# Optimization experiments

Measured on AMD Instinct MI355X. Metric: run time of the kernel, lower is better.

The kernel has to match this reference:

```python
import jax, jax.numpy as jnp
import numpy as np

N, F, E, G, NNZ = 16000, 128, 256000, 512, 512000


def _hconv(xin, row, col, hw_passed, W, b, n_nodes, n_edges):
    """PyG HypergraphConv (use_attention=False), faithful to the repo's call.
    xin: [n_nodes, Fin]; row=hyper_edge[0] (graph-edge ids), col=hyper_edge[1] (hyperedge ids).
    hw_passed: [NNZ] -- the repo passes node_weight[hyper_edge[1]]; PyG then indexes it
    again by hyperedge_index[1], so the effective per-incidence weight is hw_passed[col].
    """
    xw = xin @ W                                   # lin(x), bias=False in PyG
    w = hw_passed[col]                             # [NNZ]
    D = jax.ops.segment_sum(w, row, num_segments=n_nodes)
    Dinv = jnp.where(D == 0, 0.0, 1.0 / jnp.where(D == 0, 1.0, D))
    Bdeg = jax.ops.segment_sum(jnp.ones(row.shape, xw.dtype), col, num_segments=n_edges)
    Binv = jnp.where(Bdeg == 0, 0.0, 1.0 / jnp.where(Bdeg == 0, 1.0, Bdeg))
    # node -> hyperedge: message = B[col] * xw[row], sum over col
    out_e = jax.ops.segment_sum(Binv[col][:, None] * xw[row], col, num_segments=n_edges)
    # hyperedge -> node: message = D[row] * out_e[col], sum over row
    out = jax.ops.segment_sum(Dinv[row][:, None] * out_e[col], row, num_segments=n_nodes)
    return out + b


def setup_inputs() -> dict:
    key = jax.random.key(0)
    ks = jax.random.split(key, 20)
    rn = lambda k, shape, s=0.05: jax.random.normal(k, shape, dtype=jnp.float32) * s
    return {
        "x": jax.random.normal(ks[0], (N, F), dtype=jnp.float32),
        "graph_emb": jax.random.normal(ks[1], (G, F), dtype=jnp.float32),
        "edge_index": jax.random.randint(ks[2], (2, E), 0, N),
        "edge_type": jax.random.randint(ks[3], (E,), 0, 8),
        "batch": jnp.sort(jax.random.randint(ks[4], (N,), 0, G)),
        "hyper_edge": jnp.concatenate([
            jax.random.randint(ks[5], (1, NNZ), 0, E),   # graph-edge ids
            jax.random.randint(ks[6], (1, NNZ), 0, N)],  # hyperedge ids
            axis=0),
        # HyperWeight.lin: 2F -> F -> 1
        "hw_w1": rn(ks[7], (2 * F, F)), "hw_b1": jnp.zeros((F,), jnp.float32),
        "hw_w2": rn(ks[8], (F, 1)), "hw_b2": jnp.zeros((1,), jnp.float32),
        # HypergraphConv 1: 2F -> 2F; 2: 2F -> F (lin bias=False, separate out bias)
        "c1_w": rn(ks[9], (2 * F, 2 * F)), "c1_b": jnp.zeros((2 * F,), jnp.float32),
        "c2_w": rn(ks[10], (2 * F, F)), "c2_b": jnp.zeros((F,), jnp.float32),
        # Generator.lin: 3F -> 4F -> F
        "g_w1": rn(ks[11], (3 * F, 4 * F)), "g_b1": jnp.zeros((4 * F,), jnp.float32),
        "g_w2": rn(ks[12], (4 * F, F)), "g_b2": jnp.zeros((F,), jnp.float32),
        # classifier: 2F -> F -> 1
        "cl_w1": rn(ks[13], (2 * F, F)), "cl_b1": jnp.zeros((F,), jnp.float32),
        "cl_w2": rn(ks[14], (F, 1)), "cl_b2": jnp.zeros((1,), jnp.float32),
        "attn": jnp.array([0.5, 0.5], jnp.float32),
    }


def reference(x, graph_emb, edge_index, edge_type, batch, hyper_edge,
              hw_w1, hw_b1, hw_w2, hw_b2, c1_w, c1_b, c2_w, c2_b,
              g_w1, g_b1, g_w2, g_b2, cl_w1, cl_b1, cl_w2, cl_b2, attn):
    col, row = edge_index[0], edge_index[1]
    xij0 = jnp.concatenate([x[col], x[row]], axis=-1)          # [E, 2F]
    gemb = graph_emb[batch[edge_index[0]]]                     # [E, F] (unbatch_gemb)
    proto = graph_emb[batch]                                   # [N, F]
    # HyperWeight: per-node scalar weight
    h = jax.nn.relu(jnp.concatenate([x, proto], axis=-1) @ hw_w1 + hw_b1)
    node_w = jax.nn.sigmoid(h @ hw_w2 + hw_b2)[:, 0]           # [N]
    hrow, hcol = hyper_edge[0], hyper_edge[1]
    hw_passed = node_w[hcol]                                   # [NNZ], as in repo
    er = jax.nn.sigmoid(_hconv(xij0, hrow, hcol, hw_passed, c1_w, c1_b, E, N))
    sij = jax.nn.sigmoid(_hconv(er, hrow, hcol, hw_passed, c2_w, c2_b, E, N))  # [E, F]
    # Generator.lin on [xij, gemb]
    xl = jax.nn.relu(jnp.concatenate([xij0, gemb], axis=-1) @ g_w1 + g_b1)
    xl = jax.nn.relu(xl @ g_w2 + g_b2)                         # [E, F]
    s = attn[0] * xl + attn[1] * sij
    s = jnp.concatenate([s, gemb], axis=-1)                    # [E, 2F]
    s = jax.nn.relu(s @ cl_w1 + cl_b1)
    sij_out = jax.nn.sigmoid(s @ cl_w2 + cl_b2)                # [E, 1] (eval mode)
    return sij_out
```

## Files before the change

### kernel.cpp

```cpp
#include <hip/hip_runtime.h>
#include <hip/hip_bf16.h>
#include <hip/hip_fp16.h>

#define NODES  16000
#define FDIM   128
#define EDGES  256000
#define NNZ_   512000

typedef __attribute__((ext_vector_type(8))) short bf16x8;
typedef __attribute__((ext_vector_type(8))) _Float16 f16x8;
typedef __attribute__((ext_vector_type(4))) float f32x4;

__device__ __forceinline__ float sigmoidf_(float z) { return 1.f / (1.f + __expf(-z)); }
__device__ __forceinline__ float bflo(unsigned u) { return __uint_as_float(u << 16); }
__device__ __forceinline__ float bfhi(unsigned u) { return __uint_as_float(u & 0xffff0000u); }
__device__ __forceinline__ unsigned pack2(float lo, float hi) {
    __hip_bfloat162 h;
    h.x = __float2bfloat16(lo);
    h.y = __float2bfloat16(hi);
    return *(unsigned*)&h;
}
__device__ __forceinline__ unsigned pk_add_f16(unsigned a, unsigned b) {
    unsigned r; asm("v_pk_add_f16 %0, %1, %2" : "=v"(r) : "v"(a), "v"(b)); return r;
}
__device__ __forceinline__ unsigned pk_relu_f16(unsigned a) {
    unsigned r; asm("v_pk_max_f16 %0, %1, %2" : "=v"(r) : "v"(a), "v"(0u)); return r;
}
__device__ __forceinline__ unsigned pkh(float lo, float hi) {
    __half2 h = __floats2half2_rn(lo, hi);
    return *(unsigned*)&h;
}
__device__ __forceinline__ float2 h2f2(unsigned u) {
    return __half22float2(*(__half2*)&u);
}

__global__ __launch_bounds__(128) void hyperweight_k(
    const float* __restrict__ x, const float* __restrict__ ge, const int* __restrict__ batch,
    const float* __restrict__ w1, const float* __restrict__ b1,
    const float* __restrict__ w2, const float* __restrict__ b2, float* __restrict__ node_w)
{
    __shared__ float a[8][256];
    __shared__ float red[128];
    const int t = threadIdx.x;
    const int nb = blockIdx.x * 8;
    for (int u = 0; u < 8; ++u) {
        int n = nb + u;
        a[u][t]       = x[(size_t)n * FDIM + t];
        a[u][128 + t] = ge[(size_t)batch[n] * FDIM + t];
    }
    __syncthreads();
    float acc[8] = {0,0,0,0,0,0,0,0};
    for (int k = 0; k < 256; ++k) {
        float wv = w1[k * 128 + t];
        #pragma unroll
        for (int u = 0; u < 8; ++u) acc[u] += a[u][k] * wv;
    }
    const float wv2 = w2[t];
    for (int u = 0; u < 8; ++u) {
        float h = fmaxf(acc[u] + b1[t], 0.f);
        red[t] = h * wv2;
        __syncthreads();
        for (int s2 = 64; s2 > 0; s2 >>= 1) {
            if (t < s2) red[t] += red[t + s2];
            __syncthreads();
        }
        if (t == 0) node_w[nb + u] = sigmoidf_(red[0] + b2[0]);
        __syncthreads();
    }
}

__global__ void incidence_pass(const int* __restrict__ he, const float* __restrict__ node_w,
                               float* __restrict__ D, int* __restrict__ Bcnt, int* __restrict__ rowCnt)
{
    int i = blockIdx.x * 256 + threadIdx.x;
    if (i >= NNZ_) return;
    int hr = he[i];
    int hc = he[NNZ_ + i];
    int hc2 = he[NNZ_ + hc];
    atomicAdd(&D[hr], node_w[hc2]);
    atomicAdd(&Bcnt[hc], 1);
    atomicAdd(&rowCnt[hr], 1);
}

__global__ void inv_k(float* __restrict__ D, const int* __restrict__ Bcnt, float* __restrict__ Binv) {
    int i = blockIdx.x * 256 + threadIdx.x;
    if (i < EDGES) {
        float d = D[i];
        D[i] = (d != 0.f) ? 1.f / d : 0.f;
    }
    if (i < NODES) {
        int c = Bcnt[i];
        Binv[i] = c ? 1.f / (float)c : 0.f;
    }
}

__global__ __launch_bounds__(1024) void reduce_chunks(const int* __restrict__ in, int* __restrict__ part, int n) {
    __shared__ int s[1024];
    int t = threadIdx.x, g = blockIdx.x * 1024 + t;
    s[t] = (g < n) ? in[g] : 0;
    __syncthreads();
    for (int d = 512; d > 0; d >>= 1) {
        if (t < d) s[t] += s[t + d];
        __syncthreads();
    }
    if (t == 0) part[blockIdx.x] = s[0];
}
__global__ __launch_bounds__(1024) void scan_sums(int* __restrict__ part, int nc) {
    __shared__ int s[1024];
    int t = threadIdx.x;
    int v = (t < nc) ? part[t] : 0;
    s[t] = v;
    __syncthreads();
    for (int d = 1; d < 1024; d <<= 1) {
        int tv = (t >= d) ? s[t - d] : 0;
        __syncthreads();
        s[t] += tv;
        __syncthreads();
    }
    if (t < nc) part[t] = s[t] - v;
}
__global__ __launch_bounds__(1024) void scan_chunks(const int* __restrict__ in, const int* __restrict__ part,
                                                    int* __restrict__ out, int n) {
    __shared__ int s[1024];
    int t = threadIdx.x, g = blockIdx.x * 1024 + t;
    int v = (g < n) ? in[g] : 0;
    s[t] = v;
    __syncthreads();
    for (int d = 1; d < 1024; d <<= 1) {
        int tv = (t >= d) ? s[t - d] : 0;
        __syncthreads();
        s[t] += tv;
        __syncthreads();
    }
    int excl = s[t] - v + part[blockIdx.x];
    if (g < n) out[g] = excl;
    if (g == n - 1) out[n] = excl + v;
}

__global__ void scatter_pass(const int* __restrict__ he, const int* __restrict__ colOff, const int* __restrict__ rowOff,
                             int* __restrict__ colCur, int* __restrict__ rowCur,
                             int* __restrict__ colList, int* __restrict__ rowList)
{
    int i = blockIdx.x * 256 + threadIdx.x;
    if (i >= NNZ_) return;
    int hr = he[i];
    int hc = he[NNZ_ + i];
    int p = colOff[hc] + atomicAdd(&colCur[hc], 1);
    colList[p] = hr;
    int q = rowOff[hr] + atomicAdd(&rowCur[hr], 1);
    rowList[q] = hc;
}

__global__ void conv_x(const float* __restrict__ in, __hip_bfloat16* __restrict__ ob,
                       _Float16* __restrict__ oh, int n) {
    int i = blockIdx.x * 256 + threadIdx.x;
    if (i < n) { float v = in[i]; ob[i] = __float2bfloat16(v); oh[i] = (_Float16)v; }
}
__global__ void conv_f16(const float* __restrict__ in, _Float16* __restrict__ out, int n) {
    int i = blockIdx.x * 256 + threadIdx.x;
    if (i < n) out[i] = (_Float16)in[i];
}
__global__ void transpose_f16(const float* __restrict__ in, _Float16* __restrict__ out, int K, int N) {
    int i = blockIdx.x * 256 + threadIdx.x;
    if (i >= K * N) return;
    int n = i / K, k = i - n * K;
    out[i] = (_Float16)in[k * N + n];
}

__global__ __launch_bounds__(128) void col_gather_x(
    const __hip_bfloat16* __restrict__ xb, const int* __restrict__ ei,
    const int* __restrict__ colOff, const int* __restrict__ colList, float* __restrict__ agg)
{
    int n = blockIdx.x;
    int t = threadIdx.x;
    int base = (t < 64) ? 0 : EDGES;
    int f = t & 63;
    const unsigned* x32 = (const unsigned*)xb;
    int s = colOff[n], e = colOff[n + 1];
    float vx = 0.f, vy = 0.f;
    int j = s;
    for (; j + 3 < e; j += 4) {
        int r0 = colList[j], r1 = colList[j + 1], r2 = colList[j + 2], r3 = colList[j + 3];
        unsigned q0 = x32[(size_t)ei[base + r0] * 64 + f];
        unsigned q1 = x32[(size_t)ei[base + r1] * 64 + f];
        unsigned q2 = x32[(size_t)ei[base + r2] * 64 + f];
        unsigned q3 = x32[(size_t)ei[base + r3] * 64 + f];
        vx += bflo(q0) + bflo(q1) + bflo(q2) + bflo(q3);
        vy += bfhi(q0) + bfhi(q1) + bfhi(q2) + bfhi(q3);
    }
    for (; j < e; ++j) {
        unsigned q0 = x32[(size_t)ei[base + colList[j]] * 64 + f];
        vx += bflo(q0); vy += bfhi(q0);
    }
    int ob = (t < 64) ? 0 : 128;
    float2 o = make_float2(vx, vy);
    *(float2*)(agg + (size_t)n * 256 + ob + 2 * f) = o;
}

__global__ __launch_bounds__(128) void er_k(
    const __hip_bfloat16* __restrict__ oe1, const int* __restrict__ rowOff,
    const int* __restrict__ rowList, const float* __restrict__ Dinv,
    const float* __restrict__ c1b, __hip_bfloat16* __restrict__ er)
{
    int r = blockIdx.x;
    int t = threadIdx.x;
    int s = rowOff[r], e = rowOff[r + 1];
    const unsigned* o32 = (const unsigned*)oe1;
    float vx = 0.f, vy = 0.f;
    int j = s;
    for (; j + 1 < e; j += 2) {
        unsigned q0 = o32[(size_t)rowList[j] * 128 + t];
        unsigned q1 = o32[(size_t)rowList[j + 1] * 128 + t];
        vx += bflo(q0) + bflo(q1);
        vy += bfhi(q0) + bfhi(q1);
    }
    if (j < e) {
        unsigned q0 = o32[(size_t)rowList[j] * 128 + t];
        vx += bflo(q0); vy += bfhi(q0);
    }
    float dv = Dinv[r];
    *(unsigned*)(er + (size_t)r * 256 + 2 * t) =
        pack2(sigmoidf_(dv * vx + c1b[2 * t]), sigmoidf_(dv * vy + c1b[2 * t + 1]));
}

__global__ __launch_bounds__(128) void col_agg_er(
    const __hip_bfloat16* __restrict__ er, const int* __restrict__ colOff,
    const int* __restrict__ colList, float* __restrict__ agg)
{
    int n = blockIdx.x;
    int t = threadIdx.x;
    const unsigned* e32 = (const unsigned*)er;
    int s = colOff[n], e = colOff[n + 1];
    float vx = 0.f, vy = 0.f;
    int j = s;
    for (; j + 3 < e; j += 4) {
        unsigned q0 = e32[(size_t)colList[j]     * 128 + t];
        unsigned q1 = e32[(size_t)colList[j + 1] * 128 + t];
        unsigned q2 = e32[(size_t)colList[j + 2] * 128 + t];
        unsigned q3 = e32[(size_t)colList[j + 3] * 128 + t];
        vx += bflo(q0) + bflo(q1) + bflo(q2) + bflo(q3);
        vy += bfhi(q0) + bfhi(q1) + bfhi(q2) + bfhi(q3);
    }
    for (; j < e; ++j) {
        unsigned q0 = e32[(size_t)colList[j] * 128 + t];
        vx += bflo(q0); vy += bfhi(q0);
    }
    float2 o = make_float2(vx, vy);
    *(float2*)(agg + (size_t)n * 256 + 2 * t) = o;
}

template<int K, int NN, bool OB16>
__global__ __launch_bounds__(256) void gemm_node(
    const float* __restrict__ A, const float* __restrict__ B,
    const float* __restrict__ rowscale, void* __restrict__ C)
{
    __shared__ float As[16][68];
    __shared__ float Bs[16][68];
    const int tid = threadIdx.x;
    const int m0 = blockIdx.x * 64, n0 = blockIdx.y * 64;
    const int la_k = tid & 15, la_m = tid >> 4;
    const int lb_n = tid & 63, lb_k = tid >> 6;
    const int tn = tid & 15, tm = tid >> 4;
    float acc[4][4] = {};
    for (int k0 = 0; k0 < K; k0 += 16) {
        #pragma unroll
        for (int r = 0; r < 4; ++r)
            As[la_k][la_m + 16 * r] = A[(size_t)(m0 + la_m + 16 * r) * K + k0 + la_k];
        #pragma unroll
        for (int r = 0; r < 4; ++r)
            Bs[lb_k + 4 * r][lb_n] = B[(size_t)(k0 + lb_k + 4 * r) * NN + n0 + lb_n];
        __syncthreads();
        #pragma unroll
        for (int kk = 0; kk < 16; ++kk) {
            float4 av = *(const float4*)&As[kk][tm * 4];
            float4 bv = *(const float4*)&Bs[kk][tn * 4];
            float am[4] = {av.x, av.y, av.z, av.w};
            float bn[4] = {bv.x, bv.y, bv.z, bv.w};
            #pragma unroll
            for (int i = 0; i < 4; ++i)
                #pragma unroll
                for (int j = 0; j < 4; ++j)
                    acc[i][j] += am[i] * bn[j];
        }
        __syncthreads();
    }
    #pragma unroll
    for (int i = 0; i < 4; ++i) {
        int m = m0 + tm * 4 + i;
        float rs = rowscale[m];
        if constexpr (OB16) {
            __hip_bfloat16* Cp = (__hip_bfloat16*)C + (size_t)m * NN + n0 + tn * 4;
            #pragma unroll
            for (int j = 0; j < 4; ++j) Cp[j] = __float2bfloat16(rs * acc[i][j]);
        } else {
            float4 o = make_float4(rs * acc[i][0], rs * acc[i][1], rs * acc[i][2], rs * acc[i][3]);
            *(float4*)((float*)C + (size_t)m * NN + n0 + tn * 4) = o;
        }
    }
}

template<int LDB, bool XAG>
__global__ __launch_bounds__(256) void xw_f16(
    const _Float16* __restrict__ A, const _Float16* __restrict__ Bt, _Float16* __restrict__ dst,
    const _Float16* __restrict__ gct, const int* __restrict__ batch, const float* __restrict__ bias)
{
    __shared__ __align__(16) _Float16 As[64][40];
    __shared__ __align__(16) _Float16 Bs[128][40];
    const int tid = threadIdx.x;
    const int m0 = blockIdx.x * 64, n0 = blockIdx.y * 128;
    const int wave = tid >> 6, lane = tid & 63;
    const int wr = wave >> 1, wc = wave & 1;
    const int srow = tid >> 2, kseg = (tid & 3) * 8;
    const int nr = tid >> 1, kb = (tid & 1) * 16;
    const int fr = lane & 15, krow = (lane >> 4) * 8, rq = lane >> 4;

    f32x4 acc[2][4] = {};
    for (int k0 = 0; k0 < 128; k0 += 32) {
        *(uint4*)&As[srow][kseg] = *(const uint4*)(A + (size_t)(m0 + srow) * 128 + k0 + kseg);
        *(uint4*)&Bs[nr][kb]     = *(const uint4*)(Bt + (size_t)(n0 + nr) * LDB + k0 + kb);
        *(uint4*)&Bs[nr][kb + 8] = *(const uint4*)(Bt + (size_t)(n0 + nr) * LDB + k0 + kb + 8);
        __syncthreads();
        f16x8 af[2], bf[4];
        #pragma unroll
        for (int i = 0; i < 2; ++i) af[i] = *(const f16x8*)&As[wr * 32 + i * 16 + fr][krow];
        #pragma unroll
        for (int j = 0; j < 4; ++j) bf[j] = *(const f16x8*)&Bs[wc * 64 + j * 16 + fr][krow];
        #pragma unroll
        for (int i = 0; i < 2; ++i)
            #pragma unroll
            for (int j = 0; j < 4; ++j)
                acc[i][j] = __builtin_amdgcn_mfma_f32_16x16x32_f16(af[i], bf[j], acc[i][j], 0, 0, 0);
        __syncthreads();
    }
    #pragma unroll
    for (int i = 0; i < 2; ++i)
        #pragma unroll
        for (int j = 0; j < 4; ++j) {
            int col = n0 + wc * 64 + j * 16 + fr;
            #pragma unroll
            for (int r = 0; r < 4; ++r) {
                int row = m0 + wr * 32 + i * 16 + rq * 4 + r;
                float v = acc[i][j][r];
                if constexpr (XAG)
                    v += (float)gct[(size_t)batch[row] * 512 + col] + bias[col];
                dst[(size_t)row * 512 + col] = (_Float16)v;
            }
        }
}

__global__ __launch_bounds__(256) void gencls_mfma(
    const _Float16* __restrict__ xag, const _Float16* __restrict__ xb2,
    const _Float16* __restrict__ gw2t, const float* __restrict__ gb2,
    const _Float16* __restrict__ geh, const float* __restrict__ attn,
    const _Float16* __restrict__ clw1t, const float* __restrict__ clb1,
    const float* __restrict__ w2, const float* __restrict__ b2, const float* __restrict__ c2b,
    const __hip_bfloat16* __restrict__ oe2,
    const int* __restrict__ ei, const int* __restrict__ batch,
    const int* __restrict__ rowOff, const int* __restrict__ rowList, const float* __restrict__ Dinv,
    float* __restrict__ out)
{
    __shared__ __align__(16) _Float16 As[64][40];
    __shared__ __align__(16) _Float16 Bs[128][40];
    __shared__ __align__(16) _Float16 xlt[64][128];
    const int tid = threadIdx.x;
    const int m0 = blockIdx.x * 64;
    const int wave = tid >> 6, lane = tid & 63;
    const int wr = wave >> 1, wc = wave & 1;
    const int srow = tid >> 2, kseg = (tid & 3) * 8;
    const int nr = tid >> 1, kb = (tid & 1) * 16;
    const int fr = lane & 15, krow = (lane >> 4) * 8, rq = lane >> 4;

    const int eg = m0 + srow;
    const int cnode = ei[eg];
    const _Float16* pa = xag + (size_t)cnode * 512;
    const _Float16* pb = xb2 + (size_t)ei[EDGES + eg] * 512;
    const int gi = batch[cnode];
    const int rs = rowOff[eg], re = rowOff[eg + 1];
    const float dv = Dinv[eg];

    f32x4 acc[2][4] = {};
    for (int k0 = 0; k0 < 512; k0 += 32) {
        int kg = k0 + kseg;
        uint4 ua = *(const uint4*)(pa + kg);
        uint4 ub = *(const uint4*)(pb + kg);
        uint4 av;
        av.x = pk_relu_f16(pk_add_f16(ua.x, ub.x));
        av.y = pk_relu_f16(pk_add_f16(ua.y, ub.y));
        av.z = pk_relu_f16(pk_add_f16(ua.z, ub.z));
        av.w = pk_relu_f16(pk_add_f16(ua.w, ub.w));
        *(uint4*)&As[srow][kseg] = av;
        *(uint4*)&Bs[nr][kb]     = *(const uint4*)(gw2t + (size_t)nr * 512 + k0 + kb);
        *(uint4*)&Bs[nr][kb + 8] = *(const uint4*)(gw2t + (size_t)nr * 512 + k0 + kb + 8);
        __syncthreads();
        f16x8 af[2], bf[4];
        #pragma unroll
        for (int i = 0; i < 2; ++i) af[i] = *(const f16x8*)&As[wr * 32 + i * 16 + fr][krow];
        #pragma unroll
        for (int j = 0; j < 4; ++j) bf[j] = *(const f16x8*)&Bs[wc * 64 + j * 16 + fr][krow];
        #pragma unroll
        for (int i = 0; i < 2; ++i)
            #pragma unroll
            for (int j = 0; j < 4; ++j)
                acc[i][j] = __builtin_amdgcn_mfma_f32_16x16x32_f16(af[i], bf[j], acc[i][j], 0, 0, 0);
        __syncthreads();
    }
    #pragma unroll
    for (int i = 0; i < 2; ++i)
        #pragma unroll
        for (int j = 0; j < 4; ++j) {
            int col = wc * 64 + j * 16 + fr;
            float bc = gb2[col];
            #pragma unroll
            for (int r = 0; r < 4; ++r) {
                int row = wr * 32 + i * 16 + rq * 4 + r;
                xlt[row][col] = (_Float16)fmaxf(acc[i][j][r] + bc, 0.f);
            }
        }
    __syncthreads();

    const float a0 = attn[0], a1 = attn[1];
    f32x4 acc2[8] = {};
    for (int it = 0; it < 8; ++it) {
        int k0 = it * 32, kg = k0 + kseg;
        uint4 av;
        if (kg < 128) {
            uint4 u = *(const uint4*)&xlt[srow][kg];
            float s0 = 0.f, s1 = 0.f, s2 = 0.f, s3 = 0.f, s4 = 0.f, s5 = 0.f, s6 = 0.f, s7 = 0.f;
            for (int q = rs; q < re; ++q) {
                uint4 o = *(const uint4*)(oe2 + (size_t)rowList[q] * 128 + kg);
                s0 += bflo(o.x); s1 += bfhi(o.x); s2 += bflo(o.y); s3 += bfhi(o.y);
                s4 += bflo(o.z); s5 += bfhi(o.z); s6 += bflo(o.w); s7 += bfhi(o.w);
            }
            float4 c0 = *(const float4*)(c2b + kg);
            float4 c1 = *(const float4*)(c2b + kg + 4);
            float2 f0 = h2f2(u.x), f1 = h2f2(u.y), f2 = h2f2(u.z), f3 = h2f2(u.w);
            av.x = pkh(a0 * f0.x + a1 * sigmoidf_(dv * s0 + c0.x),
                       a0 * f0.y + a1 * sigmoidf_(dv * s1 + c0.y));
            av.y = pkh(a0 * f1.x + a1 * sigmoidf_(dv * s2 + c0.z),
                       a0 * f1.y + a1 * sigmoidf_(dv * s3 + c0.w));
            av.z = pkh(a0 * f2.x + a1 * sigmoidf_(dv * s4 + c1.x),
                       a0 * f2.y + a1 * sigmoidf_(dv * s5 + c1.y));
            av.w = pkh(a0 * f3.x + a1 * sigmoidf_(dv * s6 + c1.z),
                       a0 * f3.y + a1 * sigmoidf_(dv * s7 + c1.w));
        } else {
            av = *(const uint4*)(geh + (size_t)gi * 128 + kg - 128);
        }
        *(uint4*)&As[srow][kseg] = av;
        *(uint4*)&Bs[nr][kb]     = *(const uint4*)(clw1t + (size_t)nr * 256 + k0 + kb);
        *(uint4*)&Bs[nr][kb + 8] = *(const uint4*)(clw1t + (size_t)nr * 256 + k0 + kb + 8);
        __syncthreads();
        f16x8 af = *(const f16x8*)&As[wave * 16 + fr][krow];
        #pragma unroll
        for (int j = 0; j < 8; ++j) {
            f16x8 bf = *(const f16x8*)&Bs[j * 16 + fr][krow];
            acc2[j] = __builtin_amdgcn_mfma_f32_16x16x32_f16(af, bf, acc2[j], 0, 0, 0);
        }
        __syncthreads();
    }
    float rsum[4] = {0.f, 0.f, 0.f, 0.f};
    #pragma unroll
    for (int j = 0; j < 8; ++j) {
        int colg = j * 16 + fr;
        float bc = clb1[colg];
        float wv = w2[colg];
        #pragma unroll
        for (int r = 0; r < 4; ++r)
            rsum[r] += fmaxf(acc2[j][r] + bc, 0.f) * wv;
    }
    #pragma unroll
    for (int m = 1; m < 16; m <<= 1) {
        #pragma unroll
        for (int r = 0; r < 4; ++r) rsum[r] += __shfl_xor(rsum[r], m, 64);
    }
    if (fr == 0) {
        float bb = b2[0];
        #pragma unroll
        for (int r = 0; r < 4; ++r)
            out[m0 + wave * 16 + rq * 4 + r] = sigmoidf_(rsum[r] + bb);
    }
}

extern "C" void kernel_launch(void* const* d_in, const int* in_sizes, int n_in,
                              void* d_out, int out_size, void* d_ws, size_t ws_size,
                              hipStream_t stream)
{
    const float* x     = (const float*)d_in[0];
    const float* ge    = (const float*)d_in[1];
    const int*   ei    = (const int*)d_in[2];
    const int*   batch = (const int*)d_in[4];
    const int*   he    = (const int*)d_in[5];
    const float* hw_w1 = (const float*)d_in[6];
    const float* hw_b1 = (const float*)d_in[7];
    const float* hw_w2 = (const float*)d_in[8];
    const float* hw_b2 = (const float*)d_in[9];
    const float* c1_w  = (const float*)d_in[10];
    const float* c1_b  = (const float*)d_in[11];
    const float* c2_w  = (const float*)d_in[12];
    const float* c2_b  = (const float*)d_in[13];
    const float* g_w1  = (const float*)d_in[14];
    const float* g_b1  = (const float*)d_in[15];
    const float* g_w2  = (const float*)d_in[16];
    const float* g_b2  = (const float*)d_in[17];
    const float* cl_w1 = (const float*)d_in[18];
    const float* cl_b1 = (const float*)d_in[19];
    const float* cl_w2 = (const float*)d_in[20];
    const float* cl_b2 = (const float*)d_in[21];
    const float* attn  = (const float*)d_in[22];
    float* out = (float*)d_out;

    char* ws = (char*)d_ws;
    size_t off = 0;
    auto alloc = [&](size_t nb) -> void* {
        off = (off + 255) & ~(size_t)255;
        void* p = ws + off;
        off += nb;
        return p;
    };
    float* D      = (float*)alloc((size_t)EDGES * 4);
    int*   Bcnt   = (int*)  alloc((size_t)NODES * 4);
    int*   rowCnt = (int*)  alloc((size_t)EDGES * 4);
    int*   colCur = (int*)  alloc((size_t)NODES * 4);
    int*   rowCur = (int*)  alloc((size_t)EDGES * 4);
    size_t zero_end = off;
    float* node_w = (float*)alloc((size_t)NODES * 4);
    float* Binv   = (float*)alloc((size_t)NODES * 4);
    int*   colOff = (int*)  alloc((size_t)(NODES + 1) * 4);
    int*   rowOff = (int*)  alloc((size_t)(EDGES + 1) * 4);
    int*   colList= (int*)  alloc((size_t)NNZ_ * 4);
    int*   rowList= (int*)  alloc((size_t)NNZ_ * 4);
    int*   partA  = (int*)  alloc(1024 * 4);
    int*   partB  = (int*)  alloc(1024 * 4);
    __hip_bfloat16* xb    = (__hip_bfloat16*)alloc((size_t)NODES * FDIM * 2);
    _Float16* xh    = (_Float16*)alloc((size_t)NODES * FDIM * 2);
    _Float16* geh   = (_Float16*)alloc((size_t)512 * FDIM * 2);
    _Float16* gw1t  = (_Float16*)alloc((size_t)512 * 384 * 2);
    _Float16* gw2t  = (_Float16*)alloc((size_t)128 * 512 * 2);
    _Float16* clw1t = (_Float16*)alloc((size_t)128 * 256 * 2);
    _Float16* xag   = (_Float16*)alloc((size_t)NODES * 512 * 2);
    _Float16* xb2   = (_Float16*)alloc((size_t)NODES * 512 * 2);
    _Float16* gc    = (_Float16*)alloc((size_t)512 * 512 * 2);
    float* agg  = (float*)alloc((size_t)NODES * 256 * 4);
    __hip_bfloat16* oe1b = (__hip_bfloat16*)alloc((size_t)NODES * 256 * 2);
    __hip_bfloat16* oe2  = (__hip_bfloat16*)alloc((size_t)NODES * 128 * 2);
    __hip_bfloat16* er   = (__hip_bfloat16*)alloc((size_t)EDGES * 256 * 2);

    hipMemsetAsync(D, 0, zero_end, stream);

    hyperweight_k<<<NODES / 8, 128, 0, stream>>>(x, ge, batch, hw_w1, hw_b1, hw_w2, hw_b2, node_w);
    incidence_pass<<<NNZ_ / 256, 256, 0, stream>>>(he, node_w, D, Bcnt, rowCnt);
    inv_k<<<EDGES / 256, 256, 0, stream>>>(D, Bcnt, Binv);

    const int ncN = (NODES + 1023) / 1024;
    const int ncE = (EDGES + 1023) / 1024;
    reduce_chunks<<<ncN, 1024, 0, stream>>>(Bcnt, partA, NODES);
    scan_sums<<<1, 1024, 0, stream>>>(partA, ncN);
    scan_chunks<<<ncN, 1024, 0, stream>>>(Bcnt, partA, colOff, NODES);
    reduce_chunks<<<ncE, 1024, 0, stream>>>(rowCnt, partB, EDGES);
    scan_sums<<<1, 1024, 0, stream>>>(partB, ncE);
    scan_chunks<<<ncE, 1024, 0, stream>>>(rowCnt, partB, rowOff, EDGES);
    scatter_pass<<<NNZ_ / 256, 256, 0, stream>>>(he, colOff, rowOff, colCur, rowCur, colList, rowList);

    conv_x<<<(NODES * FDIM + 255) / 256, 256, 0, stream>>>(x, xb, xh, NODES * FDIM);
    conv_f16<<<(512 * FDIM + 255) / 256, 256, 0, stream>>>(ge, geh, 512 * FDIM);
    transpose_f16<<<(384 * 512 + 255) / 256, 256, 0, stream>>>(g_w1, gw1t, 384, 512);
    transpose_f16<<<(512 * 128 + 255) / 256, 256, 0, stream>>>(g_w2, gw2t, 512, 128);
    transpose_f16<<<(256 * 128 + 255) / 256, 256, 0, stream>>>(cl_w1, clw1t, 256, 128);

    xw_f16<384, false><<<dim3(512 / 64, 4), 256, 0, stream>>>(geh, gw1t + 256, gc, nullptr, nullptr, nullptr);
    xw_f16<384, true><<<dim3(NODES / 64, 4), 256, 0, stream>>>(xh, gw1t, xag, gc, batch, g_b1);
    xw_f16<384, false><<<dim3(NODES / 64, 4), 256, 0, stream>>>(xh, gw1t + 128, xb2, nullptr, nullptr, nullptr);

    col_gather_x<<<NODES, 128, 0, stream>>>(xb, ei, colOff, colList, agg);
    gemm_node<256, 256, true><<<dim3(NODES / 64, 4), 256, 0, stream>>>(agg, c1_w, Binv, oe1b);

    er_k<<<EDGES, 128, 0, stream>>>(oe1b, rowOff, rowList, D, c1_b, er);
    col_agg_er<<<NODES, 128, 0, stream>>>(er, colOff, colList, agg);
    gemm_node<256, 128, true><<<dim3(NODES / 64, 2), 256, 0, stream>>>(agg, c2_w, Binv, oe2);

    gencls_mfma<<<EDGES / 64, 256, 0, stream>>>(xag, xb2, gw2t, g_b2, geh, attn, clw1t, cl_b1,
                                                cl_w2, cl_b2, c2_b, oe2, ei, batch,
                                                rowOff, rowList, D, out);
}
```

Measured before the change: 731.1 us.

## Load MFMA fragments directly from global memory, dropping LDS staging and barriers in gencls

Both GEMM phases of the fused generator/classifier kernel now build their MFMA A and B fragments straight from global memory in registers instead of staging tiles through shared memory. This removes the per-k-step __syncthreads pairs and the LDS round trips. The xlt tile is padded to 136 columns to cut bank conflicts. In exchange, every wave separately fetches the gathered rows and the weight fragments, so global and L2 traffic and per-lane load latency go up, and the second phase's irregular segment sums are no longer spread evenly across threads.

```diff
diff --git a/kernel.cpp b/kernel.cpp
--- a/kernel.cpp
+++ b/kernel.cpp
@@ -359,50 +359,45 @@
     const int* __restrict__ rowOff, const int* __restrict__ rowList, const float* __restrict__ Dinv,
     float* __restrict__ out)
 {
-    __shared__ __align__(16) _Float16 As[64][40];
-    __shared__ __align__(16) _Float16 Bs[128][40];
-    __shared__ __align__(16) _Float16 xlt[64][128];
+    __shared__ __align__(16) _Float16 xlt[64][136];
     const int tid = threadIdx.x;
     const int m0 = blockIdx.x * 64;
     const int wave = tid >> 6, lane = tid & 63;
     const int wr = wave >> 1, wc = wave & 1;
-    const int srow = tid >> 2, kseg = (tid & 3) * 8;
-    const int nr = tid >> 1, kb = (tid & 1) * 16;
-    const int fr = lane & 15, krow = (lane >> 4) * 8, rq = lane >> 4;
-
-    const int eg = m0 + srow;
-    const int cnode = ei[eg];
-    const _Float16* pa = xag + (size_t)cnode * 512;
-    const _Float16* pb = xb2 + (size_t)ei[EDGES + eg] * 512;
-    const int gi = batch[cnode];
-    const int rs = rowOff[eg], re = rowOff[eg + 1];
-    const float dv = Dinv[eg];
+    const int fr = lane & 15, rq = lane >> 4, krow = rq * 8;
+
+    const int e0 = m0 + wr * 32 + fr;
+    const int e1 = e0 + 16;
+    const _Float16* pa0 = xag + (size_t)ei[e0] * 512;
+    const _Float16* pb0 = xb2 + (size_t)ei[EDGES + e0] * 512;
+    const _Float16* pa1 = xag + (size_t)ei[e1] * 512;
+    const _Float16* pb1 = xb2 + (size_t)ei[EDGES + e1] * 512;
+    const _Float16* pw1 = gw2t + (size_t)(wc * 64 + fr) * 512;
 
     f32x4 acc[2][4] = {};
     for (int k0 = 0; k0 < 512; k0 += 32) {
-        int kg = k0 + kseg;
-        uint4 ua = *(const uint4*)(pa + kg);
-        uint4 ub = *(const uint4*)(pb + kg);
-        uint4 av;
-        av.x = pk_relu_f16(pk_add_f16(ua.x, ub.x));
-        av.y = pk_relu_f16(pk_add_f16(ua.y, ub.y));
-        av.z = pk_relu_f16(pk_add_f16(ua.z, ub.z));
-        av.w = pk_relu_f16(pk_add_f16(ua.w, ub.w));
-        *(uint4*)&As[srow][kseg] = av;
-        *(uint4*)&Bs[nr][kb]     = *(const uint4*)(gw2t + (size_t)nr * 512 + k0 + kb);
-        *(uint4*)&Bs[nr][kb + 8] = *(const uint4*)(gw2t + (size_t)nr * 512 + k0 + kb + 8);
-        __syncthreads();
-        f16x8 af[2], bf[4];
-        #pragma unroll
-        for (int i = 0; i < 2; ++i) af[i] = *(const f16x8*)&As[wr * 32 + i * 16 + fr][krow];
-        #pragma unroll
-        for (int j = 0; j < 4; ++j) bf[j] = *(const f16x8*)&Bs[wc * 64 + j * 16 + fr][krow];
-        #pragma unroll
-        for (int i = 0; i < 2; ++i)
-            #pragma unroll
-            for (int j = 0; j < 4; ++j)
-                acc[i][j] = __builtin_amdgcn_mfma_f32_16x16x32_f16(af[i], bf[j], acc[i][j], 0, 0, 0);
-        __syncthreads();
+        int kg = k0 + krow;
+        uint4 ua0 = *(const uint4*)(pa0 + kg);
+        uint4 ub0 = *(const uint4*)(pb0 + kg);
+        uint4 ua1 = *(const uint4*)(pa1 + kg);
+        uint4 ub1 = *(const uint4*)(pb1 + kg);
+        uint4 f0, f1;
+        f0.x = pk_relu_f16(pk_add_f16(ua0.x, ub0.x));
+        f0.y = pk_relu_f16(pk_add_f16(ua0.y, ub0.y));
+        f0.z = pk_relu_f16(pk_add_f16(ua0.z, ub0.z));
+        f0.w = pk_relu_f16(pk_add_f16(ua0.w, ub0.w));
+        f1.x = pk_relu_f16(pk_add_f16(ua1.x, ub1.x));
+        f1.y = pk_relu_f16(pk_add_f16(ua1.y, ub1.y));
+        f1.z = pk_relu_f16(pk_add_f16(ua1.z, ub1.z));
+        f1.w = pk_relu_f16(pk_add_f16(ua1.w, ub1.w));
+        f16x8 af0 = *(f16x8*)&f0;
+        f16x8 af1 = *(f16x8*)&f1;
+        #pragma unroll
+        for (int j = 0; j < 4; ++j) {
+            f16x8 bf = *(const f16x8*)(pw1 + (size_t)j * 16 * 512 + kg);
+            acc[0][j] = __builtin_amdgcn_mfma_f32_16x16x32_f16(af0, bf, acc[0][j], 0, 0, 0);
+            acc[1][j] = __builtin_amdgcn_mfma_f32_16x16x32_f16(af1, bf, acc[1][j], 0, 0, 0);
+        }
     }
     #pragma unroll
     for (int i = 0; i < 2; ++i)
@@ -419,12 +414,19 @@
     __syncthreads();
 
     const float a0 = attn[0], a1 = attn[1];
+    const int row_l = wave * 16 + fr;
+    const int e2 = m0 + row_l;
+    const int gi = batch[ei[e2]];
+    const int rs = rowOff[e2], re = rowOff[e2 + 1];
+    const float dv = Dinv[e2];
+    const _Float16* pw2 = clw1t + (size_t)fr * 256;
+
     f32x4 acc2[8] = {};
     for (int it = 0; it < 8; ++it) {
-        int k0 = it * 32, kg = k0 + kseg;
-        uint4 av;
-        if (kg < 128) {
-            uint4 u = *(const uint4*)&xlt[srow][kg];
+        int kg = it * 32 + krow;
+        f16x8 af;
+        if (it < 4) {
+            uint4 u = *(const uint4*)&xlt[row_l][kg];
             float s0 = 0.f, s1 = 0.f, s2 = 0.f, s3 = 0.f, s4 = 0.f, s5 = 0.f, s6 = 0.f, s7 = 0.f;
             for (int q = rs; q < re; ++q) {
                 uint4 o = *(const uint4*)(oe2 + (size_t)rowList[q] * 128 + kg);
@@ -433,29 +435,25 @@
             }
             float4 c0 = *(const float4*)(c2b + kg);
             float4 c1 = *(const float4*)(c2b + kg + 4);
-            float2 f0 = h2f2(u.x), f1 = h2f2(u.y), f2 = h2f2(u.z), f3 = h2f2(u.w);
-            av.x = pkh(a0 * f0.x + a1 * sigmoidf_(dv * s0 + c0.x),
-                       a0 * f0.y + a1 * sigmoidf_(dv * s1 + c0.y));
-            av.y = pkh(a0 * f1.x + a1 * sigmoidf_(dv * s2 + c0.z),
-                       a0 * f1.y + a1 * sigmoidf_(dv * s3 + c0.w));
-            av.z = pkh(a0 * f2.x + a1 * sigmoidf_(dv * s4 + c1.x),
-                       a0 * f2.y + a1 * sigmoidf_(dv * s5 + c1.y));
-            av.w = pkh(a0 * f3.x + a1 * sigmoidf_(dv * s6 + c1.z),
-                       a0 * f3.y + a1 * sigmoidf_(dv * s7 + c1.w));
+            float2 g0 = h2f2(u.x), g1 = h2f2(u.y), g2 = h2f2(u.z), g3 = h2f2(u.w);
+            uint4 av;
+            av.x = pkh(a0 * g0.x + a1 * sigmoidf_(dv * s0 + c0.x),
+                       a0 * g0.y + a1 * sigmoidf_(dv * s1 + c0.y));
+            av.y = pkh(a0 * g1.x + a1 * sigmoidf_(dv * s2 + c0.z),
+                       a0 * g1.y + a1 * sigmoidf_(dv * s3 + c0.w));
+            av.z = pkh(a0 * g2.x + a1 * sigmoidf_(dv * s4 + c1.x),
+                       a0 * g2.y + a1 * sigmoidf_(dv * s5 + c1.y));
+            av.w = pkh(a0 * g3.x + a1 * sigmoidf_(dv * s6 + c1.z),
+                       a0 * g3.y + a1 * sigmoidf_(dv * s7 + c1.w));
+            af = *(f16x8*)&av;
         } else {
-            av = *(const uint4*)(geh + (size_t)gi * 128 + kg - 128);
-        }
-        *(uint4*)&As[srow][kseg] = av;
-        *(uint4*)&Bs[nr][kb]     = *(const uint4*)(clw1t + (size_t)nr * 256 + k0 + kb);
-        *(uint4*)&Bs[nr][kb + 8] = *(const uint4*)(clw1t + (size_t)nr * 256 + k0 + kb + 8);
-        __syncthreads();
-        f16x8 af = *(const f16x8*)&As[wave * 16 + fr][krow];
+            af = *(const f16x8*)(geh + (size_t)gi * 128 + kg - 128);
+        }
         #pragma unroll
         for (int j = 0; j < 8; ++j) {
-            f16x8 bf = *(const f16x8*)&Bs[j * 16 + fr][krow];
+            f16x8 bf = *(const f16x8*)(pw2 + (size_t)j * 16 * 256 + kg);
             acc2[j] = __builtin_amdgcn_mfma_f32_16x16x32_f16(af, bf, acc2[j], 0, 0, 0);
         }
-        __syncthreads();
     }
     float rsum[4] = {0.f, 0.f, 0.f, 0.f};
     #pragma unroll
```

Result: slower. 937.9 us (+28.3%).

## Sort edges by source node via counting-sort permutation for gencls gather locality

Applied to the files above, without the earlier changes.

Builds a permutation of edges grouped by ei[0] (counting via atomics in inv_k, scan, scatter) and makes gencls_mfma process edges in that order, writing outputs through the permutation. Blocks then share source-node rows of xag and batch/graph embeddings, which is meant to improve cache reuse on the 512-wide f16 row gathers. It also pads the xlt shared array to 136 columns to reduce LDS bank conflicts. Costs are extra scan/scatter kernels, scattered output writes, and less locality for the rowList/oe2 and xb2 gathers that follow edge order.

```diff
diff --git a/kernel.cpp b/kernel.cpp
--- a/kernel.cpp
+++ b/kernel.cpp
@@ -82,11 +82,13 @@
     atomicAdd(&rowCnt[hr], 1);
 }
 
-__global__ void inv_k(float* __restrict__ D, const int* __restrict__ Bcnt, float* __restrict__ Binv) {
+__global__ void inv_k(float* __restrict__ D, const int* __restrict__ Bcnt, float* __restrict__ Binv,
+                      const int* __restrict__ ei, int* __restrict__ ecnt) {
     int i = blockIdx.x * 256 + threadIdx.x;
     if (i < EDGES) {
         float d = D[i];
         D[i] = (d != 0.f) ? 1.f / d : 0.f;
+        atomicAdd(&ecnt[ei[i]], 1);
     }
     if (i < NODES) {
         int c = Bcnt[i];
@@ -149,6 +151,16 @@
     colList[p] = hr;
     int q = rowOff[hr] + atomicAdd(&rowCur[hr], 1);
     rowList[q] = hc;
+}
+
+__global__ void edge_scatter(const int* __restrict__ ei, const int* __restrict__ eoff,
+                             int* __restrict__ ecur, int* __restrict__ perm)
+{
+    int e = blockIdx.x * 256 + threadIdx.x;
+    if (e >= EDGES) return;
+    int c = ei[e];
+    int pos = eoff[c] + atomicAdd(&ecur[c], 1);
+    perm[pos] = e;
 }
 
 __global__ void conv_x(const float* __restrict__ in, __hip_bfloat16* __restrict__ ob,
@@ -357,20 +369,21 @@
     const __hip_bfloat16* __restrict__ oe2,
     const int* __restrict__ ei, const int* __restrict__ batch,
     const int* __restrict__ rowOff, const int* __restrict__ rowList, const float* __restrict__ Dinv,
+    const int* __restrict__ perm,
     float* __restrict__ out)
 {
     __shared__ __align__(16) _Float16 As[64][40];
     __shared__ __align__(16) _Float16 Bs[128][40];
-    __shared__ __align__(16) _Float16 xlt[64][128];
+    __shared__ __align__(16) _Float16 xlt[64][136];
     const int tid = threadIdx.x;
     const int m0 = blockIdx.x * 64;
     const int wave = tid >> 6, lane = tid & 63;
     const int wr = wave >> 1, wc = wave & 1;
     const int srow = tid >> 2, kseg = (tid & 3) * 8;
     const int nr = tid >> 1, kb = (tid & 1) * 16;
-    const int fr = lane & 15, krow = (lane >> 4) * 8, rq = lane >> 4;
-
-    const int eg = m0 + srow;
+    const int fr = lane & 15, rq = lane >> 4, krow = rq * 8;
+
+    const int eg = perm[m0 + srow];
     const int cnode = ei[eg];
     const _Float16* pa = xag + (size_t)cnode * 512;
     const _Float16* pb = xb2 + (size_t)ei[EDGES + eg] * 512;
@@ -433,15 +446,15 @@
             }
             float4 c0 = *(const float4*)(c2b + kg);
             float4 c1 = *(const float4*)(c2b + kg + 4);
-            float2 f0 = h2f2(u.x), f1 = h2f2(u.y), f2 = h2f2(u.z), f3 = h2f2(u.w);
-            av.x = pkh(a0 * f0.x + a1 * sigmoidf_(dv * s0 + c0.x),
-                       a0 * f0.y + a1 * sigmoidf_(dv * s1 + c0.y));
-            av.y = pkh(a0 * f1.x + a1 * sigmoidf_(dv * s2 + c0.z),
-                       a0 * f1.y + a1 * sigmoidf_(dv * s3 + c0.w));
-            av.z = pkh(a0 * f2.x + a1 * sigmoidf_(dv * s4 + c1.x),
-                       a0 * f2.y + a1 * sigmoidf_(dv * s5 + c1.y));
-            av.w = pkh(a0 * f3.x + a1 * sigmoidf_(dv * s6 + c1.z),
-                       a0 * f3.y + a1 * sigmoidf_(dv * s7 + c1.w));
+            float2 g0 = h2f2(u.x), g1 = h2f2(u.y), g2 = h2f2(u.z), g3 = h2f2(u.w);
+            av.x = pkh(a0 * g0.x + a1 * sigmoidf_(dv * s0 + c0.x),
+                       a0 * g0.y + a1 * sigmoidf_(dv * s1 + c0.y));
+            av.y = pkh(a0 * g1.x + a1 * sigmoidf_(dv * s2 + c0.z),
+                       a0 * g1.y + a1 * sigmoidf_(dv * s3 + c0.w));
+            av.z = pkh(a0 * g2.x + a1 * sigmoidf_(dv * s4 + c1.x),
+                       a0 * g2.y + a1 * sigmoidf_(dv * s5 + c1.y));
+            av.w = pkh(a0 * g3.x + a1 * sigmoidf_(dv * s6 + c1.z),
+                       a0 * g3.y + a1 * sigmoidf_(dv * s7 + c1.w));
         } else {
             av = *(const uint4*)(geh + (size_t)gi * 128 + kg - 128);
         }
@@ -476,7 +489,7 @@
         float bb = b2[0];
         #pragma unroll
         for (int r = 0; r < 4; ++r)
-            out[m0 + wave * 16 + rq * 4 + r] = sigmoidf_(rsum[r] + bb);
+            out[perm[m0 + wave * 16 + rq * 4 + r]] = sigmoidf_(rsum[r] + bb);
     }
 }
 
@@ -521,15 +534,20 @@
     int*   rowCnt = (int*)  alloc((size_t)EDGES * 4);
     int*   colCur = (int*)  alloc((size_t)NODES * 4);
     int*   rowCur = (int*)  alloc((size_t)EDGES * 4);
+    int*   ecnt   = (int*)  alloc((size_t)NODES * 4);
+    int*   ecur   = (int*)  alloc((size_t)NODES * 4);
     size_t zero_end = off;
     float* node_w = (float*)alloc((size_t)NODES * 4);
     float* Binv   = (float*)alloc((size_t)NODES * 4);
     int*   colOff = (int*)  alloc((size_t)(NODES + 1) * 4);
     int*   rowOff = (int*)  alloc((size_t)(EDGES + 1) * 4);
+    int*   eoff   = (int*)  alloc((size_t)(NODES + 1) * 4);
     int*   colList= (int*)  alloc((size_t)NNZ_ * 4);
     int*   rowList= (int*)  alloc((size_t)NNZ_ * 4);
+    int*   perm   = (int*)  alloc((size_t)EDGES * 4);
     int*   partA  = (int*)  alloc(1024 * 4);
     int*   partB  = (int*)  alloc(1024 * 4);
+    int*   partC  = (int*)  alloc(1024 * 4);
     __hip_bfloat16* xb    = (__hip_bfloat16*)alloc((size_t)NODES * FDIM * 2);
     _Float16* xh    = (_Float16*)alloc((size_t)NODES * FDIM * 2);
     _Float16* geh   = (_Float16*)alloc((size_t)512 * FDIM * 2);
@@ -548,7 +566,7 @@
 
     hyperweight_k<<<NODES / 8, 128, 0, stream>>>(x, ge, batch, hw_w1, hw_b1, hw_w2, hw_b2, node_w);
     incidence_pass<<<NNZ_ / 256, 256, 0, stream>>>(he, node_w, D, Bcnt, rowCnt);
-    inv_k<<<EDGES / 256, 256, 0, stream>>>(D, Bcnt, Binv);
+    inv_k<<<EDGES / 256, 256, 0, stream>>>(D, Bcnt, Binv, ei, ecnt);
 
     const int ncN = (NODES + 1023) / 1024;
     const int ncE = (EDGES + 1023) / 1024;
@@ -560,6 +578,11 @@
     scan_chunks<<<ncE, 1024, 0, stream>>>(rowCnt, partB, rowOff, EDGES);
     scatter_pass<<<NNZ_ / 256, 256, 0, stream>>>(he, colOff, rowOff, colCur, rowCur, colList, rowList);
 
+    reduce_chunks<<<ncN, 1024, 0, stream>>>(ecnt, partC, NODES);
+    scan_sums<<<1, 1024, 0, stream>>>(partC, ncN);
+    scan_chunks<<<ncN, 1024, 0, stream>>>(ecnt, partC, eoff, NODES);
+    edge_scatter<<<EDGES / 256, 256, 0, stream>>>(ei, eoff, ecur, perm);
+
     conv_x<<<(NODES * FDIM + 255) / 256, 256, 0, stream>>>(x, xb, xh, NODES * FDIM);
     conv_f16<<<(512 * FDIM + 255) / 256, 256, 0, stream>>>(ge, geh, 512 * FDIM);
     transpose_f16<<<(384 * 512 + 255) / 256, 256, 0, stream>>>(g_w1, gw1t, 384, 512);
@@ -579,5 +602,5 @@
 
     gencls_mfma<<<EDGES / 64, 256, 0, stream>>>(xag, xb2, gw2t, g_b2, geh, attn, clw1t, cl_b1,
                                                 cl_w2, cl_b2, c2_b, oe2, ei, batch,
-                                                rowOff, rowList, D, out);
-}
+                                                rowOff, rowList, D, perm, out);
+}
```

After: 764.4 us. 4.5% more time.
